# Kernel optimization log

Measured on AMD Instinct MI355X. Metric: run time of the kernel, lower is better.

Reference implementation:

```python
import jax, jax.numpy as jnp
import numpy as np

N_BINS = 15
NUM_CLASSES = 16


def _risk_from_H2(u):
    # torch: 0.5*(1 - sqrt(clamp(2*2^-u - 1, min=0)))
    inner = 2.0 * jnp.exp2(-u) - 1.0
    pos = inner > 0.0
    s = jnp.sqrt(jnp.where(pos, inner, 1.0))  # safe sqrt (grad 0 where clamped)
    return 0.5 * (1.0 - jnp.where(pos, s, 0.0))


def setup_inputs() -> dict:
    key = jax.random.key(0)
    k1, k2 = jax.random.split(key)
    N = 4194304
    logits = jax.random.normal(k1, (N, NUM_CLASSES), dtype=jnp.float32)
    labels = jax.random.randint(k2, (N,), 0, NUM_CLASSES)
    return {"logits": logits, "labels": labels}


def reference(logits, labels):
    # logits: [N, C]; labels: [N]
    probs = jax.nn.softmax(logits, axis=-1)                     # [N, C]
    H2 = -jnp.log2((probs * probs).sum(-1) + 1e-12)             # [N]
    err_real = (jnp.argmax(probs, axis=-1) != labels).astype(H2.dtype)  # [N]

    # equal-frequency edges on detached H2 (linear-interp quantiles, as torch.quantile)
    q = jnp.linspace(0.0, 1.0, N_BINS + 1)
    edges = jnp.quantile(jax.lax.stop_gradient(H2), q)
    edges = edges.at[-1].add(1e-6)
    lo, hi = edges[:-1], edges[1:]                              # [n_bins]

    # vectorized replacement of the per-bin Python loop: [n_bins, N] mask
    mask = (H2[None, :] > lo[:, None]) & (H2[None, :] <= hi[:, None])
    maskf = mask.astype(H2.dtype)
    cnt = maskf.sum(-1)                                         # [n_bins]
    safe = jnp.maximum(cnt, 1.0)
    u_bar = (maskf @ H2) / safe                                 # masked means
    err_bar = (maskf @ err_real) / safe
    gaps = jnp.where(cnt > 0.0, jnp.abs(err_bar - _risk_from_H2(u_bar)), 0.0)
    return gaps.mean()
```

## Files before the change

kernel.cpp:

```cpp
#include <hip/hip_runtime.h>

#define L1_BINS 8192
#define L2_BINS 512
#define KEY_MAX 4194303u
#define NH2_BLOCKS 1024
#define NBIN_BLOCKS 256

struct Ranks { unsigned int r[32]; };
struct Fracs { float f[16]; };

__global__ __launch_bounds__(256) void k_zero(uint4* __restrict__ p, int n4) {
  int i = blockIdx.x * blockDim.x + threadIdx.x;
  if (i < n4) p[i] = make_uint4(0u, 0u, 0u, 0u);
}

__global__ __launch_bounds__(256) void k_h2(const float* __restrict__ logits,
                                            const int* __restrict__ labels,
                                            unsigned int* __restrict__ keys,
                                            unsigned int* __restrict__ histg,
                                            int n) {
  __shared__ unsigned int lh[L1_BINS];
  for (int i = threadIdx.x; i < L1_BINS; i += blockDim.x) lh[i] = 0u;
  __syncthreads();
  int stride = gridDim.x * blockDim.x;
  for (int row = blockIdx.x * blockDim.x + threadIdx.x; row < n; row += stride) {
    const float4* rp = reinterpret_cast<const float4*>(logits) + (size_t)row * 4;
    float4 f0 = rp[0], f1 = rp[1], f2 = rp[2], f3 = rp[3];
    float l[16] = {f0.x, f0.y, f0.z, f0.w, f1.x, f1.y, f1.z, f1.w,
                   f2.x, f2.y, f2.z, f2.w, f3.x, f3.y, f3.z, f3.w};
    float m = l[0]; int am = 0;
#pragma unroll
    for (int j = 1; j < 16; ++j) { bool g = l[j] > m; m = g ? l[j] : m; am = g ? j : am; }
    float Z = 0.f, S2 = 0.f;
#pragma unroll
    for (int j = 0; j < 16; ++j) { float e = __expf(l[j] - m); Z += e; S2 += e * e; }
    float r = S2 / (Z * Z) + 1e-12f;
    float h2 = -__log2f(r);
    int ki = (int)(h2 * 1048576.0f);
    unsigned int key = (unsigned int)min(max(ki, 0), (int)KEY_MAX);
    unsigned int err = (am != labels[row]) ? 0x80000000u : 0u;
    keys[row] = key | err;
    atomicAdd(&lh[key >> 9], 1u);
  }
  __syncthreads();
  unsigned int* dst = histg + (size_t)blockIdx.x * (L1_BINS / 2);
  for (int i = threadIdx.x; i < L1_BINS / 2; i += blockDim.x)
    dst[i] = (lh[2 * i] & 0xFFFFu) | (lh[2 * i + 1] << 16);
}

__global__ __launch_bounds__(256) void k_merge(const unsigned int* __restrict__ histg,
                                               unsigned int* __restrict__ merged,
                                               int nblocks) {
  int i = blockIdx.x * blockDim.x + threadIdx.x;
  if (i < L1_BINS / 2) {
    unsigned int slo = 0, shi = 0;
    for (int b = 0; b < nblocks; ++b) {
      unsigned int v = histg[(size_t)b * (L1_BINS / 2) + i];
      slo += v & 0xFFFFu;
      shi += v >> 16;
    }
    merged[2 * i] = slo;
    merged[2 * i + 1] = shi;
  }
}

__global__ void k_select(const unsigned int* __restrict__ hist,
                         unsigned int* __restrict__ selpfx,
                         unsigned int* __restrict__ selrank,
                         float* __restrict__ vout,
                         int nb, int perq, int shift, int last, int first,
                         Ranks rk) {
  int j = blockIdx.x;
  int lane = threadIdx.x;
  const unsigned int* h = hist + (perq ? (size_t)j * (size_t)nb : (size_t)0);
  unsigned int rem = first ? rk.r[j] : selrank[j];
  int base = 0, len = nb;
  while (len > 64) {
    int chunk = (len + 63) >> 6;
    int start = base + lane * chunk;
    int end = base + len;
    unsigned int s = 0;
    for (int t = 0; t < chunk; ++t) {
      int idx = start + t;
      if (idx < end) s += h[idx];
    }
    unsigned int inc = s;
#pragma unroll
    for (int d = 1; d < 64; d <<= 1) {
      unsigned int u = __shfl_up(inc, d);
      if (lane >= d) inc += u;
    }
    unsigned int ex = inc - s;
    bool own = (rem >= ex) && (rem < ex + s);
    unsigned long long bal = __ballot(own);
    int src = __ffsll((long long)bal) - 1;
    unsigned int exs = __shfl(ex, src);
    int nbase = base + src * chunk;
    len = min(chunk, end - nbase);
    base = nbase;
    rem -= exs;
  }
  unsigned int s = (lane < len) ? h[base + lane] : 0u;
  unsigned int inc = s;
#pragma unroll
  for (int d = 1; d < 64; d <<= 1) {
    unsigned int u = __shfl_up(inc, d);
    if (lane >= d) inc += u;
  }
  unsigned int ex = inc - s;
  bool own = (rem >= ex) && (rem < ex + s);
  unsigned long long bal = __ballot(own);
  int src = __ffsll((long long)bal) - 1;
  unsigned int exs = __shfl(ex, src);
  if (lane == 0) {
    unsigned int idx = (unsigned int)(base + src);
    unsigned int pfx = first ? idx : ((selpfx[j] << shift) | idx);
    selpfx[j] = pfx;
    selrank[j] = rem - exs;
    if (last) vout[j] = __uint_as_float(pfx);
  }
}

__global__ __launch_bounds__(256) void k_refine(const unsigned int* __restrict__ keys,
                                                const unsigned int* __restrict__ selpfx,
                                                unsigned int* __restrict__ hist2,
                                                int n) {
  __shared__ unsigned int sp[32];
  if (threadIdx.x < 32) sp[threadIdx.x] = selpfx[threadIdx.x];
  __syncthreads();
  int stride = gridDim.x * blockDim.x;
  for (int i = blockIdx.x * blockDim.x + threadIdx.x; i < n; i += stride) {
    unsigned int key = keys[i] & KEY_MAX;
    unsigned int hi = key >> 9;
    unsigned int sub = key & (L2_BINS - 1);
#pragma unroll
    for (int jj = 0; jj < 32; ++jj) {
      if (hi == sp[jj]) atomicAdd(&hist2[jj * L2_BINS + (int)sub], 1u);
    }
  }
}

__global__ __launch_bounds__(256) void k_bin(const unsigned int* __restrict__ keys,
                                             const float* __restrict__ vp,
                                             float* __restrict__ partials, int n,
                                             Fracs fr) {
  __shared__ float sedge[16];
  __shared__ float swacc[4][48];
  if (threadIdx.x < 16) {
    int i = threadIdx.x;
    unsigned int klo = __float_as_uint(vp[2 * i]);
    unsigned int khi = __float_as_uint(vp[2 * i + 1]);
    float lo = (float)(klo + 1u) * 0x1p-20f;
    float hi = (float)(khi + 1u) * 0x1p-20f;
    float f = fr.f[i];
    float e = lo * (1.0f - f) + hi * f;
    if (i == 15) e += 1e-6f;
    sedge[i] = e;
  }
  __syncthreads();
  float e[16];
#pragma unroll
  for (int j = 0; j < 16; ++j) e[j] = sedge[j];
  float cnt[15], sH[15], sE[15];
#pragma unroll
  for (int b = 0; b < 15; ++b) { cnt[b] = 0.f; sH[b] = 0.f; sE[b] = 0.f; }
  int stride = gridDim.x * blockDim.x;
  for (int i = blockIdx.x * blockDim.x + threadIdx.x; i < n; i += stride) {
    unsigned int kp = keys[i];
    float h = ((float)(kp & KEY_MAX) + 0.5f) * 0x1p-20f;
    float er = (kp & 0x80000000u) ? 1.0f : 0.0f;
    int less = 0;
#pragma unroll
    for (int j = 0; j < 16; ++j) less += (h > e[j]) ? 1 : 0;
    int bin = less - 1;
#pragma unroll
    for (int b = 0; b < 15; ++b) {
      bool m = (bin == b);
      cnt[b] += m ? 1.f : 0.f;
      sH[b] += m ? h : 0.f;
      sE[b] += m ? er : 0.f;
    }
  }
  int wid = threadIdx.x >> 6;
  int lane = threadIdx.x & 63;
#pragma unroll
  for (int b = 0; b < 15; ++b) {
    float c = cnt[b], a = sH[b], s = sE[b];
    for (int off = 32; off > 0; off >>= 1) {
      c += __shfl_xor(c, off);
      a += __shfl_xor(a, off);
      s += __shfl_xor(s, off);
    }
    if (lane == 0) {
      swacc[wid][b] = c;
      swacc[wid][15 + b] = a;
      swacc[wid][30 + b] = s;
    }
  }
  __syncthreads();
  if (threadIdx.x < 45) {
    int v = threadIdx.x;
    float s = swacc[0][v] + swacc[1][v] + swacc[2][v] + swacc[3][v];
    partials[v * NBIN_BLOCKS + blockIdx.x] = s;
  }
}

__global__ void k_final(const float* __restrict__ partials, float* __restrict__ out) {
  __shared__ float sacc[45];
  int lane = threadIdx.x;
  for (int v = 0; v < 45; ++v) {
    float s = 0.f;
    for (int b = lane; b < NBIN_BLOCKS; b += 64) s += partials[v * NBIN_BLOCKS + b];
    for (int off = 32; off > 0; off >>= 1) s += __shfl_xor(s, off);
    if (lane == 0) sacc[v] = s;
  }
  __syncthreads();
  float g = 0.f;
  if (lane < 15) {
    float c = sacc[lane], sh = sacc[15 + lane], se = sacc[30 + lane];
    float safe = fmaxf(c, 1.f);
    float u = sh / safe, eb = se / safe;
    float inner = 2.0f * exp2f(-u) - 1.0f;
    float s = (inner > 0.f) ? sqrtf(inner) : 0.f;
    float risk = 0.5f * (1.0f - s);
    g = (c > 0.f) ? fabsf(eb - risk) : 0.f;
  }
  for (int off = 32; off > 0; off >>= 1) g += __shfl_xor(g, off);
  if (lane == 0) out[0] = g * (1.0f / 15.0f);
}

extern "C" void kernel_launch(void* const* d_in, const int* in_sizes, int n_in,
                              void* d_out, int out_size, void* d_ws, size_t ws_size,
                              hipStream_t stream) {
  const float* logits = (const float*)d_in[0];
  const int* labels = (const int*)d_in[1];
  float* out = (float*)d_out;
  int n = in_sizes[1];

  char* ws = (char*)d_ws;
  size_t offKeys = 0;
  size_t offHg = (size_t)n * 4;
  size_t offMerged = offHg + (size_t)NH2_BLOCKS * (L1_BINS / 2) * 4;
  size_t offH2b = offMerged + (size_t)L1_BINS * 4;
  size_t offSelP = offH2b + 32 * L2_BINS * 4;
  size_t offSelR = offSelP + 128;
  size_t offV = offSelR + 128;
  size_t offPart = (offV + 128 + 255) & ~(size_t)255;

  unsigned int* keys = (unsigned int*)(ws + offKeys);
  unsigned int* histg = (unsigned int*)(ws + offHg);
  unsigned int* merged = (unsigned int*)(ws + offMerged);
  unsigned int* hist2 = (unsigned int*)(ws + offH2b);
  unsigned int* selp = (unsigned int*)(ws + offSelP);
  unsigned int* selr = (unsigned int*)(ws + offSelR);
  float* vp = (float*)(ws + offV);
  float* part = (float*)(ws + offPart);

  Ranks rk;
  Fracs fr;
  float nm1 = (float)(n - 1);
  for (int i = 0; i < 16; ++i) {
    float q = (i == 15) ? 1.0f : (float)i * (1.0f / 15.0f);
    float idxf = q * nm1;
    float flo = floorf(idxf);
    unsigned int klo = (unsigned int)flo;
    unsigned int khi = (unsigned int)ceilf(idxf);
    unsigned int maxi = (unsigned int)(n - 1);
    if (klo > maxi) klo = maxi;
    if (khi > maxi) khi = maxi;
    rk.r[2 * i] = klo;
    rk.r[2 * i + 1] = khi;
    fr.f[i] = idxf - flo;
  }

  k_zero<<<16, 256, 0, stream>>>((uint4*)(ws + offH2b), 32 * L2_BINS / 4);
  k_h2<<<NH2_BLOCKS, 256, 0, stream>>>(logits, labels, keys, histg, n);
  k_merge<<<(L1_BINS / 2 + 255) / 256, 256, 0, stream>>>(histg, merged, NH2_BLOCKS);
  k_select<<<32, 64, 0, stream>>>(merged, selp, selr, vp, L1_BINS, 0, 0, 0, 1, rk);
  k_refine<<<NH2_BLOCKS, 256, 0, stream>>>(keys, selp, hist2, n);
  k_select<<<32, 64, 0, stream>>>(hist2, selp, selr, vp, L2_BINS, 1, 9, 1, 0, rk);
  k_bin<<<NBIN_BLOCKS, 256, 0, stream>>>(keys, vp, part, n, fr);
  k_final<<<1, 64, 0, stream>>>(part, out);

  (void)n_in; (void)out_size; (void)ws_size;
}
```

Before: 323.1 us.

## Merge histograms via global atomics, split rows across 4 lanes, fuse final reduce

k_h2 now processes each row with four lanes, each loading one float4, and combines max/argmax and softmax sums with cross-lane shuffles. This is meant to coalesce the logits loads better and give more parallelism per row. Each block now adds its shared histogram straight into the global merged histogram with atomics, which removes the per-block packed histogram buffer and the separate k_merge pass. The final reduction moves into k_bin through a last-block-done counter, and the grid sizes change. The cost is global atomic contention on the merge and only one lane in four doing the key and histogram writes.

```diff
diff --git a/kernel.cpp b/kernel.cpp
--- a/kernel.cpp
+++ b/kernel.cpp
@@ -3,7 +3,8 @@
 #define L1_BINS 8192
 #define L2_BINS 512
 #define KEY_MAX 4194303u
-#define NH2_BLOCKS 1024
+#define NH2_BLOCKS 512
+#define NREF_BLOCKS 512
 #define NBIN_BLOCKS 256
 
 struct Ranks { unsigned int r[32]; };
@@ -17,50 +18,51 @@
 __global__ __launch_bounds__(256) void k_h2(const float* __restrict__ logits,
                                             const int* __restrict__ labels,
                                             unsigned int* __restrict__ keys,
-                                            unsigned int* __restrict__ histg,
+                                            unsigned int* __restrict__ merged,
                                             int n) {
   __shared__ unsigned int lh[L1_BINS];
   for (int i = threadIdx.x; i < L1_BINS; i += blockDim.x) lh[i] = 0u;
   __syncthreads();
-  int stride = gridDim.x * blockDim.x;
-  for (int row = blockIdx.x * blockDim.x + threadIdx.x; row < n; row += stride) {
-    const float4* rp = reinterpret_cast<const float4*>(logits) + (size_t)row * 4;
-    float4 f0 = rp[0], f1 = rp[1], f2 = rp[2], f3 = rp[3];
-    float l[16] = {f0.x, f0.y, f0.z, f0.w, f1.x, f1.y, f1.z, f1.w,
-                   f2.x, f2.y, f2.z, f2.w, f3.x, f3.y, f3.z, f3.w};
-    float m = l[0]; int am = 0;
-#pragma unroll
-    for (int j = 1; j < 16; ++j) { bool g = l[j] > m; m = g ? l[j] : m; am = g ? j : am; }
-    float Z = 0.f, S2 = 0.f;
-#pragma unroll
-    for (int j = 0; j < 16; ++j) { float e = __expf(l[j] - m); Z += e; S2 += e * e; }
-    float r = S2 / (Z * Z) + 1e-12f;
-    float h2 = -__log2f(r);
-    int ki = (int)(h2 * 1048576.0f);
-    unsigned int key = (unsigned int)min(max(ki, 0), (int)KEY_MAX);
-    unsigned int err = (am != labels[row]) ? 0x80000000u : 0u;
-    keys[row] = key | err;
-    atomicAdd(&lh[key >> 9], 1u);
-  }
-  __syncthreads();
-  unsigned int* dst = histg + (size_t)blockIdx.x * (L1_BINS / 2);
-  for (int i = threadIdx.x; i < L1_BINS / 2; i += blockDim.x)
-    dst[i] = (lh[2 * i] & 0xFFFFu) | (lh[2 * i + 1] << 16);
-}
-
-__global__ __launch_bounds__(256) void k_merge(const unsigned int* __restrict__ histg,
-                                               unsigned int* __restrict__ merged,
-                                               int nblocks) {
-  int i = blockIdx.x * blockDim.x + threadIdx.x;
-  if (i < L1_BINS / 2) {
-    unsigned int slo = 0, shi = 0;
-    for (int b = 0; b < nblocks; ++b) {
-      unsigned int v = histg[(size_t)b * (L1_BINS / 2) + i];
-      slo += v & 0xFFFFu;
-      shi += v >> 16;
-    }
-    merged[2 * i] = slo;
-    merged[2 * i + 1] = shi;
+  int tid = blockIdx.x * blockDim.x + threadIdx.x;
+  int sub = tid & 3;
+  int group = tid >> 2;
+  int ngroups = (gridDim.x * blockDim.x) >> 2;
+  for (int row = group; row < n; row += ngroups) {
+    float4 v = reinterpret_cast<const float4*>(logits)[(size_t)row * 4 + sub];
+    float m = v.x; int a = 0;
+    if (v.y > m) { m = v.y; a = 1; }
+    if (v.z > m) { m = v.z; a = 2; }
+    if (v.w > m) { m = v.w; a = 3; }
+    int gidx = sub * 4 + a;
+#pragma unroll
+    for (int mask = 1; mask <= 2; mask <<= 1) {
+      float om = __shfl_xor(m, mask);
+      int oi = __shfl_xor(gidx, mask);
+      if (om > m || (om == m && oi < gidx)) { m = om; gidx = oi; }
+    }
+    float e0 = __expf(v.x - m), e1 = __expf(v.y - m);
+    float e2 = __expf(v.z - m), e3 = __expf(v.w - m);
+    float Z = e0 + e1 + e2 + e3;
+    float S2 = e0 * e0 + e1 * e1 + e2 * e2 + e3 * e3;
+#pragma unroll
+    for (int mask = 1; mask <= 2; mask <<= 1) {
+      Z += __shfl_xor(Z, mask);
+      S2 += __shfl_xor(S2, mask);
+    }
+    if (sub == 0) {
+      float r = S2 / (Z * Z) + 1e-12f;
+      float h2 = -__log2f(r);
+      int ki = (int)(h2 * 1048576.0f);
+      unsigned int key = (unsigned int)min(max(ki, 0), (int)KEY_MAX);
+      unsigned int err = (gidx != labels[row]) ? 0x80000000u : 0u;
+      keys[row] = key | err;
+      atomicAdd(&lh[key >> 9], 1u);
+    }
+  }
+  __syncthreads();
+  for (int i = threadIdx.x; i < L1_BINS; i += blockDim.x) {
+    unsigned int v = lh[i];
+    if (v) atomicAdd(&merged[i], v);
   }
 }
 
@@ -142,10 +144,13 @@
 
 __global__ __launch_bounds__(256) void k_bin(const unsigned int* __restrict__ keys,
                                              const float* __restrict__ vp,
-                                             float* __restrict__ partials, int n,
+                                             float* __restrict__ partials,
+                                             unsigned int* __restrict__ done,
+                                             float* __restrict__ out, int n,
                                              Fracs fr) {
   __shared__ float sedge[16];
   __shared__ float swacc[4][48];
+  __shared__ unsigned int is_last;
   if (threadIdx.x < 16) {
     int i = threadIdx.x;
     unsigned int klo = __float_as_uint(vp[2 * i]);
@@ -203,30 +208,33 @@
     float s = swacc[0][v] + swacc[1][v] + swacc[2][v] + swacc[3][v];
     partials[v * NBIN_BLOCKS + blockIdx.x] = s;
   }
-}
-
-__global__ void k_final(const float* __restrict__ partials, float* __restrict__ out) {
-  __shared__ float sacc[45];
-  int lane = threadIdx.x;
-  for (int v = 0; v < 45; ++v) {
-    float s = 0.f;
-    for (int b = lane; b < NBIN_BLOCKS; b += 64) s += partials[v * NBIN_BLOCKS + b];
-    for (int off = 32; off > 0; off >>= 1) s += __shfl_xor(s, off);
-    if (lane == 0) sacc[v] = s;
-  }
-  __syncthreads();
-  float g = 0.f;
-  if (lane < 15) {
-    float c = sacc[lane], sh = sacc[15 + lane], se = sacc[30 + lane];
-    float safe = fmaxf(c, 1.f);
-    float u = sh / safe, eb = se / safe;
-    float inner = 2.0f * exp2f(-u) - 1.0f;
-    float s = (inner > 0.f) ? sqrtf(inner) : 0.f;
-    float risk = 0.5f * (1.0f - s);
-    g = (c > 0.f) ? fabsf(eb - risk) : 0.f;
-  }
-  for (int off = 32; off > 0; off >>= 1) g += __shfl_xor(g, off);
-  if (lane == 0) out[0] = g * (1.0f / 15.0f);
+  __threadfence();
+  if (threadIdx.x == 0)
+    is_last = (atomicAdd(done, 1u) == (unsigned int)gridDim.x - 1u) ? 1u : 0u;
+  __syncthreads();
+  if (is_last && threadIdx.x < 64) {
+    __shared__ float sacc[45];
+    int l = threadIdx.x;
+    for (int v = 0; v < 45; ++v) {
+      float s = 0.f;
+      for (int b = l; b < NBIN_BLOCKS; b += 64) s += partials[v * NBIN_BLOCKS + b];
+      for (int off = 32; off > 0; off >>= 1) s += __shfl_xor(s, off);
+      if (l == 0) sacc[v] = s;
+    }
+    __builtin_amdgcn_s_barrier();
+    float g = 0.f;
+    if (l < 15) {
+      float c = sacc[l], sh = sacc[15 + l], se = sacc[30 + l];
+      float safe = fmaxf(c, 1.f);
+      float u = sh / safe, eb = se / safe;
+      float inner = 2.0f * exp2f(-u) - 1.0f;
+      float s = (inner > 0.f) ? sqrtf(inner) : 0.f;
+      float risk = 0.5f * (1.0f - s);
+      g = (c > 0.f) ? fabsf(eb - risk) : 0.f;
+    }
+    for (int off = 32; off > 0; off >>= 1) g += __shfl_xor(g, off);
+    if (l == 0) out[0] = g * (1.0f / 15.0f);
+  }
 }
 
 extern "C" void kernel_launch(void* const* d_in, const int* in_sizes, int n_in,
@@ -239,18 +247,19 @@
 
   char* ws = (char*)d_ws;
   size_t offKeys = 0;
-  size_t offHg = (size_t)n * 4;
-  size_t offMerged = offHg + (size_t)NH2_BLOCKS * (L1_BINS / 2) * 4;
+  size_t offMerged = (size_t)n * 4;
   size_t offH2b = offMerged + (size_t)L1_BINS * 4;
-  size_t offSelP = offH2b + 32 * L2_BINS * 4;
+  size_t offDone = offH2b + 32 * L2_BINS * 4;
+  size_t zeroEnd = offDone + 16;
+  size_t offSelP = zeroEnd;
   size_t offSelR = offSelP + 128;
   size_t offV = offSelR + 128;
   size_t offPart = (offV + 128 + 255) & ~(size_t)255;
 
   unsigned int* keys = (unsigned int*)(ws + offKeys);
-  unsigned int* histg = (unsigned int*)(ws + offHg);
   unsigned int* merged = (unsigned int*)(ws + offMerged);
   unsigned int* hist2 = (unsigned int*)(ws + offH2b);
+  unsigned int* done = (unsigned int*)(ws + offDone);
   unsigned int* selp = (unsigned int*)(ws + offSelP);
   unsigned int* selr = (unsigned int*)(ws + offSelR);
   float* vp = (float*)(ws + offV);
@@ -273,14 +282,13 @@
     fr.f[i] = idxf - flo;
   }
 
-  k_zero<<<16, 256, 0, stream>>>((uint4*)(ws + offH2b), 32 * L2_BINS / 4);
-  k_h2<<<NH2_BLOCKS, 256, 0, stream>>>(logits, labels, keys, histg, n);
-  k_merge<<<(L1_BINS / 2 + 255) / 256, 256, 0, stream>>>(histg, merged, NH2_BLOCKS);
+  int zero4 = (int)((zeroEnd - offMerged) >> 4);
+  k_zero<<<(zero4 + 255) / 256, 256, 0, stream>>>((uint4*)(ws + offMerged), zero4);
+  k_h2<<<NH2_BLOCKS, 256, 0, stream>>>(logits, labels, keys, merged, n);
   k_select<<<32, 64, 0, stream>>>(merged, selp, selr, vp, L1_BINS, 0, 0, 0, 1, rk);
-  k_refine<<<NH2_BLOCKS, 256, 0, stream>>>(keys, selp, hist2, n);
+  k_refine<<<NREF_BLOCKS, 256, 0, stream>>>(keys, selp, hist2, n);
   k_select<<<32, 64, 0, stream>>>(hist2, selp, selr, vp, L2_BINS, 1, 9, 1, 0, rk);
-  k_bin<<<NBIN_BLOCKS, 256, 0, stream>>>(keys, vp, part, n, fr);
-  k_final<<<1, 64, 0, stream>>>(part, out);
+  k_bin<<<NBIN_BLOCKS, 256, 0, stream>>>(keys, vp, part, done, out, n, fr);
 
   (void)n_in; (void)out_size; (void)ws_size;
 }
```

Result: slower. 330.7 us (+2.4%).
